# Kernel optimization log

Measured on AMD Instinct MI355X. Metric: run time of the kernel, lower is better.

Reference implementation:

```python
import jax, jax.numpy as jnp
import numpy as np

H, DD, NCLS, NELEM, NPROP = 256, 32, 8, 11, 14
B, N = 4, 4096
ENC = NELEM + NPROP  # 25

_DIMS = [("dc1", ENC, H), ("dc21", H, DD), ("dc22", H, DD),
         ("in1", ENC, H), ("in2", H, H), ("in3", H, H),
         ("conv", H, H),
         ("id1", H, H), ("id2", H, H), ("id3", H, H),
         ("oid", H, NCLS), ("och", H, 2),
         ("m1", H + NCLS, H + NCLS), ("m2", H + NCLS, H), ("m3", H, H), ("om", H, 3)]


def setup_inputs() -> dict:
    key = jax.random.key(0)
    ks = jax.random.split(key, 2 + len(_DIMS))
    X = jax.random.normal(ks[0], (B, N, 15), jnp.float32)
    ids = jax.random.randint(ks[1], (B, N), 0, NELEM).astype(jnp.float32)
    X = X.at[:, :, 0].set(ids)
    d = {"X": X}
    for i, (name, di, do) in enumerate(_DIMS):
        W = jax.random.normal(ks[2 + i], (di, do), jnp.float32) / np.sqrt(di)
        d["W_" + name] = W
        d["b_" + name] = jnp.zeros((do,), jnp.float32)
    return d


def reference(X, W_dc1, b_dc1, W_dc21, b_dc21, W_dc22, b_dc22,
              W_in1, b_in1, W_in2, b_in2, W_in3, b_in3,
              W_conv, b_conv,
              W_id1, b_id1, W_id2, b_id2, W_id3, b_id3,
              W_oid, b_oid, W_och, b_och,
              W_m1, b_m1, W_m2, b_m2, W_m3, b_m3, W_om, b_om):
    act = jax.nn.selu
    # input encoding: one-hot element id (stop-grad via int cast) + properties, then selu
    onehot = jax.nn.one_hot(X[:, :, 0].astype(jnp.int32), NELEM, dtype=X.dtype)
    enc = act(jnp.concatenate([onehot, X[:, :, 1:]], axis=-1))  # [B,N,25]
    # distance coordinates
    h = act(enc @ W_dc1 + b_dc1)
    c1 = h @ W_dc21 + b_dc21  # [B,N,DD]
    c2 = h @ W_dc22 + b_dc22
    # pairwise distance -> exp adjacency
    na = jnp.sum(c1 * c1, -1)[:, :, None]
    nb = jnp.sum(c2 * c2, -1)[:, None, :]
    Dsq = jnp.clip(na - 2.0 * jnp.einsum('bnd,bmd->bnm', c1, c2) + nb, 1e-12, 1e12)
    adj = jnp.exp(-jnp.sqrt(Dsq))  # [B,N,N]
    # node MLP
    x = act(enc @ W_in1 + b_in1)
    x = act(x @ W_in2 + b_in2)
    x = act(x @ W_in3 + b_in3)
    # GraphConv: adj^k @ (x W) + b, k=4 (in-degree norm computed but unused upstream)
    x = act(jnp.einsum('bnm,bmh->bnh', adj ** 4, x @ W_conv) + b_conv)
    # id head
    a = act(x @ W_id1 + b_id1)
    a = act(a @ W_id2 + b_id2)
    a = act(a @ W_id3 + b_id3)
    out_id_logits = a @ W_oid + b_oid  # [B,N,8]
    out_charge = a @ W_och + b_och     # [B,N,2]
    # momentum head
    xb = jnp.concatenate([x, act(out_id_logits)], axis=-1)
    bb = act(xb @ W_m1 + b_m1)
    bb = act(bb @ W_m2 + b_m2)
    bb = act(bb @ W_m3 + b_m3)
    corr = bb @ W_om + b_om  # [B,N,3]
    mom = jnp.stack([X[:, :, 2] + corr[:, :, 0],
                     X[:, :, 3] + corr[:, :, 1],
                     X[:, :, 4] + corr[:, :, 2]], axis=-1)
    return jnp.concatenate([out_id_logits, mom, out_charge], axis=-1)  # [B,N,13]
```

## Files before the change

kernel.cpp:

```cpp
#include <hip/hip_runtime.h>
#include <cstddef>
#include <cstdint>

#define MROWS 16384
#define NSEQ  4096
#define ASTR  296
#define SELU_SCALE  1.0507009873554805f
#define SELU_ASCALE 1.7580993408473766f

typedef short bf16x8 __attribute__((ext_vector_type(8)));
typedef float f32x4  __attribute__((ext_vector_type(4)));

__device__ __forceinline__ float selu_f(float x) {
    return x > 0.f ? SELU_SCALE * x : SELU_ASCALE * (__expf(x) - 1.f);
}
__device__ __forceinline__ unsigned short f2bf(float x) {
    union { float f; unsigned int u; } v; v.f = x;
    unsigned int r = v.u + 0x7fffu + ((v.u >> 16) & 1u);
    return (unsigned short)(r >> 16);
}
__device__ __forceinline__ unsigned short t2bf(float x) {
    union { float f; unsigned int u; } v; v.f = x;
    return (unsigned short)(v.u >> 16);
}

struct PrepEnt { const float* W; unsigned short* WTf; int N, K, ntiles, KS, tileOff, tilesN; };
struct PrepArgs {
    PrepEnt e[16];
    const float *b21, *b22, *boid, *boch, *bdc1, *bin1;
    float *bc12, *boo, *bcat;
};
__global__ __launch_bounds__(256) void prep_kernel(PrepArgs pa) {
    if (blockIdx.y == 1) {
        if (blockIdx.x == 0) {
            int t = threadIdx.x;
            if (t < 32) pa.bc12[t] = pa.b21[t];
            else if (t < 64) pa.bc12[t] = pa.b22[t - 32];
            else if (t < 96) {
                int j = t - 64;
                pa.boo[j] = j < 8 ? pa.boid[j] : ((j >= 16 && j < 18) ? pa.boch[j - 16] : 0.f);
            }
        } else if (blockIdx.x == 1) {
            pa.bcat[threadIdx.x] = pa.bdc1[threadIdx.x];
        } else if (blockIdx.x == 2) {
            pa.bcat[256 + threadIdx.x] = pa.bin1[threadIdx.x];
        }
        return;
    }
    int bx = blockIdx.x;
    int ei = 0;
#pragma unroll
    for (int e = 1; e < 16; ++e)
        if (bx >= pa.e[e].tileOff) ei = e;
    PrepEnt E = pa.e[ei];
    int local = bx - E.tileOff;
    int tn = local / E.KS, tk = local - tn * E.KS;
    int k0 = tk * 32, n0 = tn * 32;

    __shared__ float ts[32][33];
    int t = threadIdx.x;
    {
        int kl = t >> 3, nl4 = (t & 7) * 4;
        int gk = k0 + kl;
#pragma unroll
        for (int j = 0; j < 4; ++j) {
            int gn = n0 + nl4 + j;
            float v = (gk < E.K && gn < E.N) ? E.W[(size_t)gk * E.N + gn] : 0.f;
            ts[nl4 + j][kl] = v;
        }
    }
    __syncthreads();
    int nl = t >> 3, kl4 = (t & 7) * 4;
    int n = n0 + nl;
    if (n < E.ntiles * 16) {
        ushort4 o;
        o.x = f2bf(ts[nl][kl4 + 0]);
        o.y = f2bf(ts[nl][kl4 + 1]);
        o.z = f2bf(ts[nl][kl4 + 2]);
        o.w = f2bf(ts[nl][kl4 + 3]);
        size_t dst = ((size_t)(n >> 4) * E.KS + tk) * 512 +
                     (size_t)((kl4 >> 3) * 16 + (n & 15)) * 8 + (kl4 & 7);
        *(ushort4*)(E.WTf + dst) = o;
    }
}

template <int MT, int NT>
__device__ __forceinline__ void zero_acc(f32x4 (&acc)[MT][NT]) {
#pragma unroll
    for (int i = 0; i < MT; ++i)
#pragma unroll
        for (int nt = 0; nt < NT; ++nt) acc[i][nt] = (f32x4){0.f, 0.f, 0.f, 0.f};
}

template <int MT, int NT, int K>
__device__ __forceinline__ void compute_tiles(
    f32x4 (&acc)[MT][NT],
    const unsigned short* __restrict__ src, int sstr,
    const unsigned short* __restrict__ WTf,
    int col0, int ln)
{
    constexpr int KS = (K + 31) / 32;
    int quad = ln >> 4, l15 = ln & 15;
    const unsigned short* wp = WTf + (size_t)(col0 >> 4) * (KS * 512) + ln * 8;
    bf16x8 st[3][NT];
#pragma unroll
    for (int s = 0; s < 3; ++s) {
        if (s < KS) {
#pragma unroll
            for (int nt = 0; nt < NT; ++nt)
                st[s][nt] = *(const bf16x8*)(wp + nt * (KS * 512) + s * 512);
        }
    }
#pragma unroll
    for (int ks = 0; ks < KS; ++ks) {
        bf16x8 bnew[NT];
        if (ks + 3 < KS) {
#pragma unroll
            for (int nt = 0; nt < NT; ++nt)
                bnew[nt] = *(const bf16x8*)(wp + nt * (KS * 512) + (ks + 3) * 512);
        }
#pragma unroll
        for (int i = 0; i < MT; ++i) {
            bf16x8 af = *(const bf16x8*)(src + (i * 16 + l15) * sstr + ks * 32 + quad * 8);
#pragma unroll
            for (int nt = 0; nt < NT; ++nt)
                acc[i][nt] = __builtin_amdgcn_mfma_f32_16x16x32_bf16(af, st[ks % 3][nt], acc[i][nt], 0, 0, 0);
        }
        if (ks + 3 < KS) {
#pragma unroll
            for (int nt = 0; nt < NT; ++nt) st[ks % 3][nt] = bnew[nt];
        }
    }
}

template <int MT, int NT>
__device__ __forceinline__ void store_tiles(
    f32x4 (&acc)[MT][NT], unsigned short* __restrict__ dst,
    int col0, const float* __restrict__ bias, int Nreal, int act, int ln)
{
    int quad = ln >> 4, l15 = ln & 15;
#pragma unroll
    for (int nt = 0; nt < NT; ++nt) {
        int col = col0 + nt * 16 + l15;
        float bv = (bias && col < Nreal) ? bias[col] : 0.f;
#pragma unroll
        for (int i = 0; i < MT; ++i) {
#pragma unroll
            for (int r = 0; r < 4; ++r) {
                int row = i * 16 + quad * 4 + r;
                float v = acc[i][nt][r] + bv;
                if (act) v = selu_f(v);
                if (col >= Nreal) v = 0.f;
                dst[row * ASTR + col] = f2bf(v);
            }
        }
    }
}

__global__ __launch_bounds__(256, 3) void pre_mega(
    const float* __restrict__ X,
    const unsigned short* __restrict__ WTdF, const float* __restrict__ bcat,
    const unsigned short* __restrict__ WTc12F, const float* __restrict__ bc12,
    const unsigned short* __restrict__ WTin2F, const float* __restrict__ b_in2,
    const unsigned short* __restrict__ WTin3F, const float* __restrict__ b_in3,
    const unsigned short* __restrict__ WTconvF,
    unsigned short* __restrict__ c1b, unsigned short* __restrict__ c2b,
    float* __restrict__ n1, float* __restrict__ n2,
    unsigned short* __restrict__ xwTb)
{
    __shared__ unsigned short encs[32 * 32];
    __shared__ unsigned short bufA[32 * ASTR];
    __shared__ unsigned short bufB[32 * ASTR];
    __shared__ float c12s[32 * 68];

    int tid = threadIdx.x, wv = tid >> 6, ln = tid & 63;
    int quad = ln >> 4, l15 = ln & 15;
    int row0 = blockIdx.x * 32;

#pragma unroll
    for (int p = 0; p < 4; ++p) {
        int idx = p * 256 + tid;
        int row = idx >> 5, col = idx & 31;
        float v = 0.f;
        if (col < 11) {
            int id = (int)X[(size_t)(row0 + row) * 15];
            v = (id == col) ? SELU_SCALE : 0.f;
        } else if (col < 25) {
            v = selu_f(X[(size_t)(row0 + row) * 15 + 1 + (col - 11)]);
        }
        encs[row * 32 + col] = f2bf(v);
    }
    __syncthreads();

#pragma unroll
    for (int ph = 0; ph < 2; ++ph) {
        f32x4 acc[2][4]; zero_acc<2, 4>(acc);
        compute_tiles<2, 4, 32>(acc, encs, 32, WTdF + (size_t)ph * 16 * 512, wv * 64, ln);
        store_tiles<2, 4>(acc, ph ? bufB : bufA, wv * 64, bcat + ph * 256, 256, 1, ln);
    }
    __syncthreads();

    f32x4 ax2[2][4]; zero_acc<2, 4>(ax2);
    compute_tiles<2, 4, 256>(ax2, bufB, ASTR, WTin2F, wv * 64, ln);
    f32x4 ac12[2][1]; zero_acc<2, 1>(ac12);
    compute_tiles<2, 1, 256>(ac12, bufA, ASTR, WTc12F, wv * 16, ln);
    __syncthreads();
    store_tiles<2, 4>(ax2, bufA, wv * 64, b_in2, 256, 1, ln);
    {
        int col = wv * 16 + l15;
        float bv = bc12[col];
#pragma unroll
        for (int i = 0; i < 2; ++i)
#pragma unroll
            for (int r = 0; r < 4; ++r)
                c12s[(i * 16 + quad * 4 + r) * 68 + col] = ac12[i][0][r] + bv;
    }
    __syncthreads();

    if (tid < 32) {
        int grow = row0 + tid;
        const float* p = &c12s[tid * 68];
        float s1 = 0.f, s2 = 0.f;
        unsigned int o1[16], o2[16];
#pragma unroll
        for (int k = 0; k < 32; k += 2) {
            float a0 = p[k], a1 = p[k + 1];
            s1 += a0 * a0 + a1 * a1;
            o1[k >> 1] = (unsigned)f2bf(a0) | ((unsigned)f2bf(a1) << 16);
            float b0 = p[32 + k], b1 = p[33 + k];
            s2 += b0 * b0 + b1 * b1;
            o2[k >> 1] = (unsigned)f2bf(b0) | ((unsigned)f2bf(b1) << 16);
        }
        uint4* d1 = (uint4*)(c1b + (size_t)grow * 32);
        uint4* d2 = (uint4*)(c2b + (size_t)grow * 32);
#pragma unroll
        for (int j = 0; j < 4; ++j) {
            d1[j] = make_uint4(o1[4 * j], o1[4 * j + 1], o1[4 * j + 2], o1[4 * j + 3]);
            d2[j] = make_uint4(o2[4 * j], o2[4 * j + 1], o2[4 * j + 2], o2[4 * j + 3]);
        }
        n1[grow] = s1;
        n2[grow] = s2;
    }

    {
        f32x4 acc[2][4]; zero_acc<2, 4>(acc);
        compute_tiles<2, 4, 256>(acc, bufA, ASTR, WTin3F, wv * 64, ln);
        store_tiles<2, 4>(acc, bufB, wv * 64, b_in3, 256, 1, ln);
    }
    __syncthreads();
    {
        f32x4 acc[2][4]; zero_acc<2, 4>(acc);
        compute_tiles<2, 4, 256>(acc, bufB, ASTR, WTconvF, wv * 64, ln);
        store_tiles<2, 4>(acc, bufA, wv * 64, nullptr, 256, 0, ln);
    }
    __syncthreads();

    int b = row0 >> 12;
    int c0 = (row0 & 4095) >> 5;
    unsigned short* dst = xwTb + (size_t)(b * 128 + c0) * (256 * 32);
#pragma unroll
    for (int p = 0; p < 4; ++p) {
        int idx = p * 256 + tid;
        int h = idx >> 2, g = idx & 3;
        unsigned int w[4];
#pragma unroll
        for (int j = 0; j < 4; ++j) {
            unsigned int lo = bufA[(g * 8 + 2 * j) * ASTR + h];
            unsigned int hi = bufA[(g * 8 + 2 * j + 1) * ASTR + h];
            w[j] = lo | (hi << 16);
        }
        *(uint4*)(dst + (size_t)h * 32 + g * 8) = make_uint4(w[0], w[1], w[2], w[3]);
    }
}

__global__ __launch_bounds__(512, 4) void adj_conv_mfma(
    const unsigned short* __restrict__ c1b, const unsigned short* __restrict__ c2b,
    const float* __restrict__ n1, const float* __restrict__ n2,
    const unsigned short* __restrict__ xwTb, const float* __restrict__ bconv,
    unsigned short* __restrict__ xc)
{
    __shared__ unsigned short wls[2][32][136];

    int tid = threadIdx.x, wv = tid >> 6, ln = tid & 63, quad = ln >> 4, l15 = ln & 15;
    int blk = blockIdx.x;
    int b = (blk >> 1) & 3;
    int iidx = ((blk >> 3) << 1) | (blk & 1);
    int i0 = iidx * 32;
    size_t base = (size_t)b * NSEQ;

    bf16x8 c1f0 = *(const bf16x8*)(c1b + (base + i0 + l15) * 32 + quad * 8);
    bf16x8 c1f1 = *(const bf16x8*)(c1b + (base + i0 + 16 + l15) * 32 + quad * 8);
    float4 n1v0 = *(const float4*)(n1 + base + i0 + quad * 4);
    float4 n1v1 = *(const float4*)(n1 + base + i0 + 16 + quad * 4);

    const unsigned short* xwp0 = xwTb + (size_t)b * (128 * 256 * 32)
                               + ((size_t)(wv * 32 + l15) * 32 + quad * 8);
    const unsigned short* xwp1 = xwp0 + 8192;
    const unsigned short* xwp2 = xwp0 + 16384;
    const unsigned short* xwp3 = xwp0 + 24576;
    const unsigned short* c2p  = c2b + (base + wv * 16 + l15) * 32 + quad * 8;
    const float* n2p = n2 + base + wv * 16 + l15;

    f32x4 acc[2][2];
#pragma unroll
    for (int i = 0; i < 2; ++i)
#pragma unroll
        for (int j = 0; j < 2; ++j) acc[i][j] = (f32x4){0.f, 0.f, 0.f, 0.f};

    bf16x8 c2f = *(const bf16x8*)c2p;
    float nn2 = *n2p;
    c2p += 4096; n2p += 128;
    {
        f32x4 d0 = (f32x4){0.f, 0.f, 0.f, 0.f};
        f32x4 d1 = (f32x4){0.f, 0.f, 0.f, 0.f};
        d0 = __builtin_amdgcn_mfma_f32_16x16x32_bf16(c1f0, c2f, d0, 0, 0, 0);
        d1 = __builtin_amdgcn_mfma_f32_16x16x32_bf16(c1f1, c2f, d1, 0, 0, 0);
#pragma unroll
        for (int r = 0; r < 4; ++r) {
            float D0 = fmaf(-2.f, d0[r], n1v0[r] + nn2);
            float D1 = fmaf(-2.f, d1[r], n1v1[r] + nn2);
            float t0 = __builtin_amdgcn_sqrtf(fmaxf(D0, 1e-12f));
            float t1 = __builtin_amdgcn_sqrtf(fmaxf(D1, 1e-12f));
            wls[0][quad * 4 + r][wv * 16 + l15]      = t2bf(__expf(t0 * -4.f));
            wls[0][16 + quad * 4 + r][wv * 16 + l15] = t2bf(__expf(t1 * -4.f));
        }
    }
    c2f = *(const bf16x8*)c2p;
    nn2 = *n2p;
    c2p += 4096; n2p += 128;
    __syncthreads();

    for (int itr = 0; itr < 32; ++itr) {
        int p = itr & 1;
        bf16x8 bfc[4][2];
#pragma unroll
        for (int ht = 0; ht < 2; ++ht) {
            bfc[0][ht] = *(const bf16x8*)(xwp0 + ht * 512);
            bfc[1][ht] = *(const bf16x8*)(xwp1 + ht * 512);
            bfc[2][ht] = *(const bf16x8*)(xwp2 + ht * 512);
            bfc[3][ht] = *(const bf16x8*)(xwp3 + ht * 512);
        }
        xwp0 += 32768; xwp1 += 32768; xwp2 += 32768; xwp3 += 32768;

        if (itr < 31) {
            f32x4 d0 = (f32x4){0.f, 0.f, 0.f, 0.f};
            f32x4 d1 = (f32x4){0.f, 0.f, 0.f, 0.f};
            d0 = __builtin_amdgcn_mfma_f32_16x16x32_bf16(c1f0, c2f, d0, 0, 0, 0);
            d1 = __builtin_amdgcn_mfma_f32_16x16x32_bf16(c1f1, c2f, d1, 0, 0, 0);
            bf16x8 c2n; float nnn;
            if (itr < 30) {
                c2n = *(const bf16x8*)c2p;
                nnn = *n2p;
                c2p += 4096; n2p += 128;
            }
#pragma unroll
            for (int r = 0; r < 4; ++r) {
                float D0 = fmaf(-2.f, d0[r], n1v0[r] + nn2);
                float D1 = fmaf(-2.f, d1[r], n1v1[r] + nn2);
                float t0 = __builtin_amdgcn_sqrtf(fmaxf(D0, 1e-12f));
                float t1 = __builtin_amdgcn_sqrtf(fmaxf(D1, 1e-12f));
                wls[p ^ 1][quad * 4 + r][wv * 16 + l15]      = t2bf(__expf(t0 * -4.f));
                wls[p ^ 1][16 + quad * 4 + r][wv * 16 + l15] = t2bf(__expf(t1 * -4.f));
            }
            if (itr < 30) { c2f = c2n; nn2 = nnn; }
        }

#pragma unroll
        for (int ks = 0; ks < 4; ++ks) {
            bf16x8 af0 = *(const bf16x8*)&wls[p][l15][ks * 32 + quad * 8];
            bf16x8 af1 = *(const bf16x8*)&wls[p][16 + l15][ks * 32 + quad * 8];
            acc[0][0] = __builtin_amdgcn_mfma_f32_16x16x32_bf16(af0, bfc[ks][0], acc[0][0], 0, 0, 0);
            acc[0][1] = __builtin_amdgcn_mfma_f32_16x16x32_bf16(af0, bfc[ks][1], acc[0][1], 0, 0, 0);
            acc[1][0] = __builtin_amdgcn_mfma_f32_16x16x32_bf16(af1, bfc[ks][0], acc[1][0], 0, 0, 0);
            acc[1][1] = __builtin_amdgcn_mfma_f32_16x16x32_bf16(af1, bfc[ks][1], acc[1][1], 0, 0, 0);
        }
        __syncthreads();
    }

#pragma unroll
    for (int mi = 0; mi < 2; ++mi) {
#pragma unroll
        for (int ht = 0; ht < 2; ++ht) {
            int h = wv * 32 + ht * 16 + l15;
            float bv = bconv[h];
#pragma unroll
            for (int r = 0; r < 4; ++r) {
                int irow = i0 + mi * 16 + quad * 4 + r;
                xc[(base + irow) * 256 + h] = f2bf(selu_f(acc[mi][ht][r] + bv));
            }
        }
    }
}

__global__ __launch_bounds__(256, 2) void post_mega(
    const float* __restrict__ X, const unsigned short* __restrict__ xc,
    const unsigned short* __restrict__ WTid1F, const float* __restrict__ b_id1,
    const unsigned short* __restrict__ WTid2F, const float* __restrict__ b_id2,
    const unsigned short* __restrict__ WTid3F, const float* __restrict__ b_id3,
    const unsigned short* __restrict__ WTooF, const float* __restrict__ boo,
    const unsigned short* __restrict__ WTm1F, const float* __restrict__ b_m1,
    const unsigned short* __restrict__ WTm2F, const float* __restrict__ b_m2,
    const unsigned short* __restrict__ WTm3F, const float* __restrict__ b_m3,
    const unsigned short* __restrict__ WTomF, const float* __restrict__ b_om,
    float* __restrict__ out)
{
    __shared__ unsigned short xcs[32 * ASTR];
    __shared__ unsigned short bufA[32 * ASTR];
    __shared__ unsigned short bufB[32 * ASTR];
    __shared__ float lgs[32 * 32];

    int tid = threadIdx.x, wv = tid >> 6, ln = tid & 63;
    int quad = ln >> 4, l15 = ln & 15;
    int row0 = blockIdx.x * 32;

#pragma unroll
    for (int p = 0; p < 4; ++p) {
        int idx = p * 256 + tid;
        int row = idx >> 5, c8 = (idx & 31) * 8;
        *(uint4*)&xcs[row * ASTR + c8] = *(const uint4*)(xc + (size_t)(row0 + row) * 256 + c8);
    }
#pragma unroll
    for (int p = 0; p < 5; ++p) {
        int idx = p * 256 + tid;
        int row = idx / 40, c = 256 + idx - row * 40;
        xcs[row * ASTR + c] = 0;
        bufB[row * ASTR + c] = 0;
    }
    __syncthreads();

    {
        f32x4 acc[2][4]; zero_acc<2, 4>(acc);
        compute_tiles<2, 4, 256>(acc, xcs, ASTR, WTid1F, wv * 64, ln);
        store_tiles<2, 4>(acc, bufA, wv * 64, b_id1, 256, 1, ln);
    }
    __syncthreads();
    {
        f32x4 acc[2][4]; zero_acc<2, 4>(acc);
        compute_tiles<2, 4, 256>(acc, bufA, ASTR, WTid2F, wv * 64, ln);
        store_tiles<2, 4>(acc, bufB, wv * 64, b_id2, 256, 1, ln);
    }
    __syncthreads();
    {
        f32x4 acc[2][4]; zero_acc<2, 4>(acc);
        compute_tiles<2, 4, 256>(acc, bufB, ASTR, WTid3F, wv * 64, ln);
        store_tiles<2, 4>(acc, bufA, wv * 64, b_id3, 256, 1, ln);
    }
    __syncthreads();
    if (wv == 0) {
        f32x4 acc[2][2]; zero_acc<2, 2>(acc);
        compute_tiles<2, 2, 256>(acc, bufA, ASTR, WTooF, 0, ln);
#pragma unroll
        for (int nt = 0; nt < 2; ++nt) {
            int col = nt * 16 + l15;
            float bv = boo[col];
#pragma unroll
            for (int i = 0; i < 2; ++i)
#pragma unroll
                for (int r = 0; r < 4; ++r)
                    lgs[(i * 16 + quad * 4 + r) * 32 + col] = acc[i][nt][r] + bv;
        }
    }
    __syncthreads();
    if (tid < 32) {
        float* op = out + (size_t)(row0 + tid) * 13;
#pragma unroll
        for (int c = 0; c < 8; ++c) {
            float lg = lgs[tid * 32 + c];
            op[c] = lg;
            xcs[tid * ASTR + 256 + c] = f2bf(selu_f(lg));
        }
        op[11] = lgs[tid * 32 + 16];
        op[12] = lgs[tid * 32 + 17];
    }
    __syncthreads();
    {
        f32x4 acc[2][4]; zero_acc<2, 4>(acc);
        compute_tiles<2, 4, 288>(acc, xcs, ASTR, WTm1F, wv * 64, ln);
        store_tiles<2, 4>(acc, bufB, wv * 64, b_m1, 264, 1, ln);
        if (wv == 1) {
            f32x4 acx[2][1]; zero_acc<2, 1>(acx);
            compute_tiles<2, 1, 288>(acx, xcs, ASTR, WTm1F, 256, ln);
            store_tiles<2, 1>(acx, bufB, 256, b_m1, 264, 1, ln);
        }
    }
    __syncthreads();
    {
        f32x4 acc[2][4]; zero_acc<2, 4>(acc);
        compute_tiles<2, 4, 288>(acc, bufB, ASTR, WTm2F, wv * 64, ln);
        store_tiles<2, 4>(acc, bufA, wv * 64, b_m2, 256, 1, ln);
    }
    __syncthreads();
    {
        f32x4 acc[2][4]; zero_acc<2, 4>(acc);
        compute_tiles<2, 4, 256>(acc, bufA, ASTR, WTm3F, wv * 64, ln);
        store_tiles<2, 4>(acc, bufB, wv * 64, b_m3, 256, 1, ln);
    }
    __syncthreads();
    if (wv == 0) {
        f32x4 acc[2][1]; zero_acc<2, 1>(acc);
        compute_tiles<2, 1, 256>(acc, bufB, ASTR, WTomF, 0, ln);
        if (l15 < 3) {
            float bv = b_om[l15];
#pragma unroll
            for (int i = 0; i < 2; ++i)
#pragma unroll
                for (int r = 0; r < 4; ++r) {
                    int grow = row0 + i * 16 + quad * 4 + r;
                    out[(size_t)grow * 13 + 8 + l15] =
                        X[(size_t)grow * 15 + 2 + l15] + acc[i][0][r] + bv;
                }
        }
    }
}

extern "C" void kernel_launch(void* const* d_in, const int* in_sizes, int n_in,
                              void* d_out, int out_size, void* d_ws, size_t ws_size,
                              hipStream_t stream) {
    (void)in_sizes; (void)n_in; (void)out_size; (void)ws_size;

    const float* X = (const float*)d_in[0];
    const float* W_dc1 = (const float*)d_in[1];  const float* b_dc1 = (const float*)d_in[2];
    const float* W_dc21 = (const float*)d_in[3]; const float* b_dc21 = (const float*)d_in[4];
    const float* W_dc22 = (const float*)d_in[5]; const float* b_dc22 = (const float*)d_in[6];
    const float* W_in1 = (const float*)d_in[7];  const float* b_in1 = (const float*)d_in[8];
    const float* W_in2 = (const float*)d_in[9];  const float* b_in2 = (const float*)d_in[10];
    const float* W_in3 = (const float*)d_in[11]; const float* b_in3 = (const float*)d_in[12];
    const float* W_conv = (const float*)d_in[13]; const float* b_conv = (const float*)d_in[14];
    const float* W_id1 = (const float*)d_in[15]; const float* b_id1 = (const float*)d_in[16];
    const float* W_id2 = (const float*)d_in[17]; const float* b_id2 = (const float*)d_in[18];
    const float* W_id3 = (const float*)d_in[19]; const float* b_id3 = (const float*)d_in[20];
    const float* W_oid = (const float*)d_in[21]; const float* b_oid = (const float*)d_in[22];
    const float* W_och = (const float*)d_in[23]; const float* b_och = (const float*)d_in[24];
    const float* W_m1 = (const float*)d_in[25];  const float* b_m1 = (const float*)d_in[26];
    const float* W_m2 = (const float*)d_in[27];  const float* b_m2 = (const float*)d_in[28];
    const float* W_m3 = (const float*)d_in[29];  const float* b_m3 = (const float*)d_in[30];
    const float* W_om = (const float*)d_in[31];  const float* b_om = (const float*)d_in[32];

    const size_t M = MROWS;
    char* pw = (char*)d_ws;
    auto alloc = [&](size_t bytes) -> void* {
        void* r = (void*)pw;
        pw += (bytes + 255) & ~(size_t)255;
        return r;
    };
    unsigned short* c1b = (unsigned short*)alloc(M * 32 * 2);
    unsigned short* c2b = (unsigned short*)alloc(M * 32 * 2);
    float* n1 = (float*)alloc(M * 4);
    float* n2 = (float*)alloc(M * 4);
    unsigned short* xwTb = (unsigned short*)alloc((size_t)4 * 128 * 256 * 32 * 2);
    unsigned short* xcb = (unsigned short*)alloc(M * 256 * 2);
    unsigned short* WTdF   = (unsigned short*)alloc((size_t)2 * 16 * 1 * 512 * 2);
    unsigned short* WTc12F = (unsigned short*)alloc((size_t)4 * 8 * 512 * 2);
    unsigned short* WTin2F = (unsigned short*)alloc((size_t)16 * 8 * 512 * 2);
    unsigned short* WTin3F = (unsigned short*)alloc((size_t)16 * 8 * 512 * 2);
    unsigned short* WTconvF = (unsigned short*)alloc((size_t)16 * 8 * 512 * 2);
    unsigned short* WTid1F = (unsigned short*)alloc((size_t)16 * 8 * 512 * 2);
    unsigned short* WTid2F = (unsigned short*)alloc((size_t)16 * 8 * 512 * 2);
    unsigned short* WTid3F = (unsigned short*)alloc((size_t)16 * 8 * 512 * 2);
    unsigned short* WTm3F  = (unsigned short*)alloc((size_t)16 * 8 * 512 * 2);
    unsigned short* WTooF  = (unsigned short*)alloc((size_t)2 * 8 * 512 * 2);
    unsigned short* WTm1F  = (unsigned short*)alloc((size_t)17 * 9 * 512 * 2);
    unsigned short* WTm2F  = (unsigned short*)alloc((size_t)16 * 9 * 512 * 2);
    unsigned short* WTomF  = (unsigned short*)alloc((size_t)1 * 8 * 512 * 2);
    float* bc12 = (float*)alloc(64 * 4);
    float* boo = (float*)alloc(32 * 4);
    float* bcat = (float*)alloc(512 * 4);

    PrepArgs pa;
    int off = 0;
    auto ent = [&](const float* W, unsigned short* WTf, int N, int K, int ntiles) {
        PrepEnt e; e.W = W; e.WTf = WTf; e.N = N; e.K = K; e.ntiles = ntiles;
        e.KS = (K + 31) / 32;
        e.tilesN = (ntiles * 16 + 31) / 32;
        e.tileOff = off;
        off += e.tilesN * e.KS;
        return e;
    };
    pa.e[0]  = ent(W_dc1,  WTdF,                256, 25,  16);
    pa.e[1]  = ent(W_in1,  WTdF + 16 * 512,     256, 25,  16);
    pa.e[2]  = ent(W_dc21, WTc12F,              32,  256, 2);
    pa.e[3]  = ent(W_dc22, WTc12F + 2 * 8 * 512, 32, 256, 2);
    pa.e[4]  = ent(W_in2,  WTin2F,              256, 256, 16);
    pa.e[5]  = ent(W_in3,  WTin3F,              256, 256, 16);
    pa.e[6]  = ent(W_conv, WTconvF,             256, 256, 16);
    pa.e[7]  = ent(W_id1,  WTid1F,              256, 256, 16);
    pa.e[8]  = ent(W_id2,  WTid2F,              256, 256, 16);
    pa.e[9]  = ent(W_id3,  WTid3F,              256, 256, 16);
    pa.e[10] = ent(W_m3,   WTm3F,               256, 256, 16);
    pa.e[11] = ent(W_oid,  WTooF,               8,   256, 1);
    pa.e[12] = ent(W_och,  WTooF + 8 * 512,     2,   256, 1);
    pa.e[13] = ent(W_m1,   WTm1F,               264, 264, 17);
    pa.e[14] = ent(W_m2,   WTm2F,               256, 264, 16);
    pa.e[15] = ent(W_om,   WTomF,               3,   256, 1);
    pa.b21 = b_dc21; pa.b22 = b_dc22; pa.boid = b_oid; pa.boch = b_och;
    pa.bdc1 = b_dc1; pa.bin1 = b_in1;
    pa.bc12 = bc12; pa.boo = boo; pa.bcat = bcat;
    prep_kernel<<<dim3(off, 2), 256, 0, stream>>>(pa);

    pre_mega<<<dim3(512), 256, 0, stream>>>(X, WTdF, bcat, WTc12F, bc12,
                                            WTin2F, b_in2, WTin3F, b_in3, WTconvF,
                                            c1b, c2b, n1, n2, xwTb);

    adj_conv_mfma<<<dim3(512), 512, 0, stream>>>(c1b, c2b, n1, n2, xwTb, b_conv, xcb);

    post_mega<<<dim3(512), 256, 0, stream>>>(X, xcb,
                                             WTid1F, b_id1, WTid2F, b_id2, WTid3F, b_id3,
                                             WTooF, boo, WTm1F, b_m1, WTm2F, b_m2,
                                             WTm3F, b_m3, WTomF, b_om, (float*)d_out);
}
```

Measured before the change: 256.0 us.

## Warp-specialize adj_conv into adjacency-producer and MFMA-consumer waves

The 8 waves of adj_conv_mfma are split into 4 producer waves and 4 consumer waves. Producers compute the exp-distance adjacency tiles, now two column tiles each, into double-buffered LDS. Consumers load xW fragments with software prefetch and run the adj@xW MFMAs over 64 output columns each. The goal is to overlap the transcendental-heavy adjacency generation with matrix-core work. In exchange, half the waves sit idle during each phase, and consumers use more accumulator registers, which may hurt occupancy at launch_bounds(512,4).

```diff
diff --git a/kernel.cpp b/kernel.cpp
--- a/kernel.cpp
+++ b/kernel.cpp
@@ -287,106 +287,131 @@
     int iidx = ((blk >> 3) << 1) | (blk & 1);
     int i0 = iidx * 32;
     size_t base = (size_t)b * NSEQ;
-
-    bf16x8 c1f0 = *(const bf16x8*)(c1b + (base + i0 + l15) * 32 + quad * 8);
-    bf16x8 c1f1 = *(const bf16x8*)(c1b + (base + i0 + 16 + l15) * 32 + quad * 8);
-    float4 n1v0 = *(const float4*)(n1 + base + i0 + quad * 4);
-    float4 n1v1 = *(const float4*)(n1 + base + i0 + 16 + quad * 4);
-
-    const unsigned short* xwp0 = xwTb + (size_t)b * (128 * 256 * 32)
-                               + ((size_t)(wv * 32 + l15) * 32 + quad * 8);
-    const unsigned short* xwp1 = xwp0 + 8192;
-    const unsigned short* xwp2 = xwp0 + 16384;
-    const unsigned short* xwp3 = xwp0 + 24576;
-    const unsigned short* c2p  = c2b + (base + wv * 16 + l15) * 32 + quad * 8;
-    const float* n2p = n2 + base + wv * 16 + l15;
-
-    f32x4 acc[2][2];
+    bool producer = (wv < 4);
+
+    f32x4 acc[2][4];
 #pragma unroll
     for (int i = 0; i < 2; ++i)
 #pragma unroll
-        for (int j = 0; j < 2; ++j) acc[i][j] = (f32x4){0.f, 0.f, 0.f, 0.f};
-
-    bf16x8 c2f = *(const bf16x8*)c2p;
-    float nn2 = *n2p;
-    c2p += 4096; n2p += 128;
-    {
-        f32x4 d0 = (f32x4){0.f, 0.f, 0.f, 0.f};
-        f32x4 d1 = (f32x4){0.f, 0.f, 0.f, 0.f};
-        d0 = __builtin_amdgcn_mfma_f32_16x16x32_bf16(c1f0, c2f, d0, 0, 0, 0);
-        d1 = __builtin_amdgcn_mfma_f32_16x16x32_bf16(c1f1, c2f, d1, 0, 0, 0);
+        for (int j = 0; j < 4; ++j) acc[i][j] = (f32x4){0.f, 0.f, 0.f, 0.f};
+
+    bf16x8 c1f0, c1f1;
+    float4 n1v0, n1v1;
+    const unsigned short* c2p = nullptr;
+    const float* n2p = nullptr;
+    int mt0 = 0;
+    const unsigned short* xwr = nullptr;
+    bf16x8 bcur[4];
+
+    if (producer) {
+        mt0 = wv * 2;
+        c1f0 = *(const bf16x8*)(c1b + (base + i0 + l15) * 32 + quad * 8);
+        c1f1 = *(const bf16x8*)(c1b + (base + i0 + 16 + l15) * 32 + quad * 8);
+        n1v0 = *(const float4*)(n1 + base + i0 + quad * 4);
+        n1v1 = *(const float4*)(n1 + base + i0 + 16 + quad * 4);
+        c2p = c2b + (base + mt0 * 16 + l15) * 32 + quad * 8;
+        n2p = n2 + base + mt0 * 16 + l15;
+
+        bf16x8 c2fa = *(const bf16x8*)c2p;
+        bf16x8 c2fb = *(const bf16x8*)(c2p + 512);
+        float nna = n2p[0], nnb = n2p[16];
+        c2p += 4096; n2p += 128;
+        f32x4 da0 = (f32x4){0.f,0.f,0.f,0.f}, da1 = da0, db0 = da0, db1 = da0;
+        da0 = __builtin_amdgcn_mfma_f32_16x16x32_bf16(c1f0, c2fa, da0, 0, 0, 0);
+        da1 = __builtin_amdgcn_mfma_f32_16x16x32_bf16(c1f1, c2fa, da1, 0, 0, 0);
+        db0 = __builtin_amdgcn_mfma_f32_16x16x32_bf16(c1f0, c2fb, db0, 0, 0, 0);
+        db1 = __builtin_amdgcn_mfma_f32_16x16x32_bf16(c1f1, c2fb, db1, 0, 0, 0);
 #pragma unroll
         for (int r = 0; r < 4; ++r) {
-            float D0 = fmaf(-2.f, d0[r], n1v0[r] + nn2);
-            float D1 = fmaf(-2.f, d1[r], n1v1[r] + nn2);
-            float t0 = __builtin_amdgcn_sqrtf(fmaxf(D0, 1e-12f));
-            float t1 = __builtin_amdgcn_sqrtf(fmaxf(D1, 1e-12f));
-            wls[0][quad * 4 + r][wv * 16 + l15]      = t2bf(__expf(t0 * -4.f));
-            wls[0][16 + quad * 4 + r][wv * 16 + l15] = t2bf(__expf(t1 * -4.f));
-        }
-    }
-    c2f = *(const bf16x8*)c2p;
-    nn2 = *n2p;
-    c2p += 4096; n2p += 128;
+            float D;
+            D = fmaf(-2.f, da0[r], n1v0[r] + nna);
+            wls[0][quad * 4 + r][mt0 * 16 + l15] = t2bf(__expf(__builtin_amdgcn_sqrtf(fmaxf(D, 1e-12f)) * -4.f));
+            D = fmaf(-2.f, da1[r], n1v1[r] + nna);
+            wls[0][16 + quad * 4 + r][mt0 * 16 + l15] = t2bf(__expf(__builtin_amdgcn_sqrtf(fmaxf(D, 1e-12f)) * -4.f));
+            D = fmaf(-2.f, db0[r], n1v0[r] + nnb);
+            wls[0][quad * 4 + r][mt0 * 16 + 16 + l15] = t2bf(__expf(__builtin_amdgcn_sqrtf(fmaxf(D, 1e-12f)) * -4.f));
+            D = fmaf(-2.f, db1[r], n1v1[r] + nnb);
+            wls[0][16 + quad * 4 + r][mt0 * 16 + 16 + l15] = t2bf(__expf(__builtin_amdgcn_sqrtf(fmaxf(D, 1e-12f)) * -4.f));
+        }
+    } else {
+        int cw = wv - 4;
+        xwr = xwTb + (size_t)b * (128 * 256 * 32)
+            + ((size_t)(cw * 64 + l15) * 32 + quad * 8);
+#pragma unroll
+        for (int nt = 0; nt < 4; ++nt)
+            bcur[nt] = *(const bf16x8*)(xwr + nt * 512);
+    }
     __syncthreads();
 
     for (int itr = 0; itr < 32; ++itr) {
         int p = itr & 1;
-        bf16x8 bfc[4][2];
-#pragma unroll
-        for (int ht = 0; ht < 2; ++ht) {
-            bfc[0][ht] = *(const bf16x8*)(xwp0 + ht * 512);
-            bfc[1][ht] = *(const bf16x8*)(xwp1 + ht * 512);
-            bfc[2][ht] = *(const bf16x8*)(xwp2 + ht * 512);
-            bfc[3][ht] = *(const bf16x8*)(xwp3 + ht * 512);
-        }
-        xwp0 += 32768; xwp1 += 32768; xwp2 += 32768; xwp3 += 32768;
-
-        if (itr < 31) {
-            f32x4 d0 = (f32x4){0.f, 0.f, 0.f, 0.f};
-            f32x4 d1 = (f32x4){0.f, 0.f, 0.f, 0.f};
-            d0 = __builtin_amdgcn_mfma_f32_16x16x32_bf16(c1f0, c2f, d0, 0, 0, 0);
-            d1 = __builtin_amdgcn_mfma_f32_16x16x32_bf16(c1f1, c2f, d1, 0, 0, 0);
-            bf16x8 c2n; float nnn;
-            if (itr < 30) {
-                c2n = *(const bf16x8*)c2p;
-                nnn = *n2p;
+        if (producer) {
+            if (itr < 31) {
+                bf16x8 c2fa = *(const bf16x8*)c2p;
+                bf16x8 c2fb = *(const bf16x8*)(c2p + 512);
+                float nna = n2p[0], nnb = n2p[16];
                 c2p += 4096; n2p += 128;
+                f32x4 da0 = (f32x4){0.f,0.f,0.f,0.f}, da1 = da0, db0 = da0, db1 = da0;
+                da0 = __builtin_amdgcn_mfma_f32_16x16x32_bf16(c1f0, c2fa, da0, 0, 0, 0);
+                da1 = __builtin_amdgcn_mfma_f32_16x16x32_bf16(c1f1, c2fa, da1, 0, 0, 0);
+                db0 = __builtin_amdgcn_mfma_f32_16x16x32_bf16(c1f0, c2fb, db0, 0, 0, 0);
+                db1 = __builtin_amdgcn_mfma_f32_16x16x32_bf16(c1f1, c2fb, db1, 0, 0, 0);
+                int q = p ^ 1;
+#pragma unroll
+                for (int r = 0; r < 4; ++r) {
+                    float D;
+                    D = fmaf(-2.f, da0[r], n1v0[r] + nna);
+                    wls[q][quad * 4 + r][mt0 * 16 + l15] = t2bf(__expf(__builtin_amdgcn_sqrtf(fmaxf(D, 1e-12f)) * -4.f));
+                    D = fmaf(-2.f, da1[r], n1v1[r] + nna);
+                    wls[q][16 + quad * 4 + r][mt0 * 16 + l15] = t2bf(__expf(__builtin_amdgcn_sqrtf(fmaxf(D, 1e-12f)) * -4.f));
+                    D = fmaf(-2.f, db0[r], n1v0[r] + nnb);
+                    wls[q][quad * 4 + r][mt0 * 16 + 16 + l15] = t2bf(__expf(__builtin_amdgcn_sqrtf(fmaxf(D, 1e-12f)) * -4.f));
+                    D = fmaf(-2.f, db1[r], n1v1[r] + nnb);
+                    wls[q][16 + quad * 4 + r][mt0 * 16 + 16 + l15] = t2bf(__expf(__builtin_amdgcn_sqrtf(fmaxf(D, 1e-12f)) * -4.f));
+                }
             }
-#pragma unroll
-            for (int r = 0; r < 4; ++r) {
-                float D0 = fmaf(-2.f, d0[r], n1v0[r] + nn2);
-                float D1 = fmaf(-2.f, d1[r], n1v1[r] + nn2);
-                float t0 = __builtin_amdgcn_sqrtf(fmaxf(D0, 1e-12f));
-                float t1 = __builtin_amdgcn_sqrtf(fmaxf(D1, 1e-12f));
-                wls[p ^ 1][quad * 4 + r][wv * 16 + l15]      = t2bf(__expf(t0 * -4.f));
-                wls[p ^ 1][16 + quad * 4 + r][wv * 16 + l15] = t2bf(__expf(t1 * -4.f));
+        } else {
+#pragma unroll
+            for (int ks = 0; ks < 4; ++ks) {
+                bf16x8 bnext[4];
+                bool last = (itr == 31) && (ks == 3);
+                if (!last) {
+                    const unsigned short* np = (ks < 3) ? (xwr + (ks + 1) * 8192)
+                                                        : (xwr + 32768);
+#pragma unroll
+                    for (int nt = 0; nt < 4; ++nt)
+                        bnext[nt] = *(const bf16x8*)(np + nt * 512);
+                }
+                bf16x8 af0 = *(const bf16x8*)&wls[p][l15][ks * 32 + quad * 8];
+                bf16x8 af1 = *(const bf16x8*)&wls[p][16 + l15][ks * 32 + quad * 8];
+#pragma unroll
+                for (int nt = 0; nt < 4; ++nt) {
+                    acc[0][nt] = __builtin_amdgcn_mfma_f32_16x16x32_bf16(af0, bcur[nt], acc[0][nt], 0, 0, 0);
+                    acc[1][nt] = __builtin_amdgcn_mfma_f32_16x16x32_bf16(af1, bcur[nt], acc[1][nt], 0, 0, 0);
+                }
+                if (!last) {
+#pragma unroll
+                    for (int nt = 0; nt < 4; ++nt) bcur[nt] = bnext[nt];
+                }
             }
-            if (itr < 30) { c2f = c2n; nn2 = nnn; }
-        }
-
-#pragma unroll
-        for (int ks = 0; ks < 4; ++ks) {
-            bf16x8 af0 = *(const bf16x8*)&wls[p][l15][ks * 32 + quad * 8];
-            bf16x8 af1 = *(const bf16x8*)&wls[p][16 + l15][ks * 32 + quad * 8];
-            acc[0][0] = __builtin_amdgcn_mfma_f32_16x16x32_bf16(af0, bfc[ks][0], acc[0][0], 0, 0, 0);
-            acc[0][1] = __builtin_amdgcn_mfma_f32_16x16x32_bf16(af0, bfc[ks][1], acc[0][1], 0, 0, 0);
-            acc[1][0] = __builtin_amdgcn_mfma_f32_16x16x32_bf16(af1, bfc[ks][0], acc[1][0], 0, 0, 0);
-            acc[1][1] = __builtin_amdgcn_mfma_f32_16x16x32_bf16(af1, bfc[ks][1], acc[1][1], 0, 0, 0);
+            xwr += 32768;
         }
         __syncthreads();
     }
 
-#pragma unroll
-    for (int mi = 0; mi < 2; ++mi) {
-#pragma unroll
-        for (int ht = 0; ht < 2; ++ht) {
-            int h = wv * 32 + ht * 16 + l15;
-            float bv = bconv[h];
-#pragma unroll
-            for (int r = 0; r < 4; ++r) {
-                int irow = i0 + mi * 16 + quad * 4 + r;
-                xc[(base + irow) * 256 + h] = f2bf(selu_f(acc[mi][ht][r] + bv));
+    if (!producer) {
+        int cw = wv - 4;
+#pragma unroll
+        for (int mi = 0; mi < 2; ++mi) {
+#pragma unroll
+            for (int nt = 0; nt < 4; ++nt) {
+                int h = cw * 64 + nt * 16 + l15;
+                float bv = bconv[h];
+#pragma unroll
+                for (int r = 0; r < 4; ++r) {
+                    int irow = i0 + mi * 16 + quad * 4 + r;
+                    xc[(base + irow) * 256 + h] = f2bf(selu_f(acc[mi][nt][r] + bv));
+                }
             }
         }
     }
```

Result: slower. 265.5 us (+3.7%).
